# Kernel optimization log

Measured on AMD Instinct MI355X. Metric: run time of the kernel, lower is better.

## Reference

```python
import jax, jax.numpy as jnp
import numpy as np

GRID = 7
NUM_CLASSES = 80
LAMBDA_COORD = 5.0
LAMBDA_NOOBJ = 0.5
EPS_IOU = 1e-06
EPS_SQRT = 1e-06


def setup_inputs() -> dict:
    key = jax.random.key(0)
    k1, k2, k3 = jax.random.split(key, 3)
    B = 4096
    D = 10 + NUM_CLASSES
    pred = jax.random.uniform(k1, (B, GRID, GRID, D), dtype=jnp.float32)
    target = jax.random.uniform(k2, (B, GRID, GRID, D), dtype=jnp.float32)
    # confidence channel of target must be exactly 1.0 for object cells
    obj = (jax.random.uniform(k3, (B, GRID, GRID)) < 0.25).astype(jnp.float32)
    target = target.at[..., 4].set(obj)
    return {"pred": pred, "target": target}


def _iou(b1, b2):
    # b1, b2: [..., 4] boxes as (cx, cy, w, h) in image coords
    x1, y1, w1, h1 = b1[..., 0], b1[..., 1], b1[..., 2], b1[..., 3]
    x2, y2, w2, h2 = b2[..., 0], b2[..., 1], b2[..., 2], b2[..., 3]
    ix_min = jnp.maximum(x1 - w1 / 2, x2 - w2 / 2)
    iy_min = jnp.maximum(y1 - h1 / 2, y2 - h2 / 2)
    ix_max = jnp.minimum(x1 + w1 / 2, x2 + w2 / 2)
    iy_max = jnp.minimum(y1 + h1 / 2, y2 + h2 / 2)
    iw = jnp.clip(ix_max - ix_min, 0.0)
    ih = jnp.clip(iy_max - iy_min, 0.0)
    inter = iw * ih
    union = w1 * h1 + w2 * h2 - inter
    return inter / (union + EPS_IOU)


def _forward(pred, target):
    S = pred.shape[1]
    gy = jnp.arange(S, dtype=pred.dtype).reshape(1, S, 1)
    gx = jnp.arange(S, dtype=pred.dtype).reshape(1, 1, S)

    def to_img(box5):  # [B,S,S,5] cell-relative -> [B,S,S,4] image coords
        cx = (gx + box5[..., 0]) / S
        cy = (gy + box5[..., 1]) / S
        return jnp.stack([cx, cy, box5[..., 2], box5[..., 3]], axis=-1)

    box1 = pred[..., 0:5]
    box2 = pred[..., 5:10]
    tbox = target[..., 0:5]

    iou1 = _iou(to_img(box1), to_img(tbox))
    iou2 = _iou(to_img(box2), to_img(tbox))
    resp1 = iou1 > iou2  # box1 responsible if strictly greater (matches `if iou1 > iou2`)
    best = jnp.where(resp1[..., None], box1, box2)  # [B,S,S,5]

    obj = target[..., 4] == 1.0  # [B,S,S]
    objf = obj.astype(pred.dtype)
    n_obj = jnp.sum(objf)
    n_cells = jnp.asarray(pred.shape[0] * S * S, pred.dtype)

    # coord: mean-of-2 xy MSE + mean-of-2 sqrt(wh) MSE per responsible box
    dxy2 = jnp.sum((best[..., 0:2] - tbox[..., 0:2]) ** 2, axis=-1)
    swh_p = jnp.sqrt(jnp.clip(best[..., 2:4], EPS_SQRT))
    swh_t = jnp.sqrt(jnp.clip(tbox[..., 2:4], EPS_SQRT))
    dwh2 = jnp.sum((swh_p - swh_t) ** 2, axis=-1)
    coord_per = 0.5 * dxy2 + 0.5 * dwh2
    coord_loss = jnp.sum(coord_per * objf) / jnp.maximum(n_obj, 1.0)

    # confidence: obj cells -> (best_conf - 1)^2 (count 1); noobj -> lam*(c1^2 + c2^2) (count 2)
    conf_obj = (best[..., 4] - 1.0) ** 2
    conf_noobj = LAMBDA_NOOBJ * (pred[..., 4] ** 2 + pred[..., 9] ** 2)
    conf_sum = jnp.sum(jnp.where(obj, conf_obj, conf_noobj))
    conf_count = n_obj + 2.0 * (n_cells - n_obj)
    conf_loss = conf_sum / jnp.maximum(conf_count, 1.0)

    # class: mean over classes per obj cell
    class_per = jnp.mean((pred[..., 10:] - target[..., 10:]) ** 2, axis=-1)
    class_loss = jnp.sum(class_per * objf) / jnp.maximum(n_obj, 1.0)

    return LAMBDA_COORD * coord_loss + conf_loss + class_loss


def reference(pred, target):
    return _forward(pred, target)
```

## Files before the change

### kernel.cpp

```cpp
#include <hip/hip_runtime.h>

#define GRID_S 7
#define NUM_CLASSES 80
#define D_DIM 90
#define LAMBDA_COORD 5.0f
#define LAMBDA_NOOBJ 0.5f
#define EPS_IOU 1e-6f
#define EPS_SQRT 1e-6f

#define GA 630

__device__ __forceinline__ float iou_img(float cx1, float cy1, float w1, float h1,
                                         float cx2, float cy2, float w2, float h2) {
    float ixmin = fmaxf(cx1 - w1 * 0.5f, cx2 - w2 * 0.5f);
    float iymin = fmaxf(cy1 - h1 * 0.5f, cy2 - h2 * 0.5f);
    float ixmax = fminf(cx1 + w1 * 0.5f, cx2 + w2 * 0.5f);
    float iymax = fminf(cy1 + h1 * 0.5f, cy2 + h2 * 0.5f);
    float iw = fmaxf(ixmax - ixmin, 0.0f);
    float ih = fmaxf(iymax - iymin, 0.0f);
    float inter = iw * ih;
    float uni = w1 * h1 + w2 * h2 - inter;
    return inter / (uni + EPS_IOU);
}

__global__ __launch_bounds__(256) void yolo_main_kernel(
        const float* __restrict__ pred, const float* __restrict__ targ,
        float* __restrict__ part, int ncells) {
    const int tid = threadIdx.x;
    float v_obj = 0.0f, v_coord = 0.0f, v_conf = 0.0f, v_cls = 0.0f;

    if (blockIdx.x < GA) {
        const int NF4 = (ncells * D_DIM) >> 2;
        const int T = GA * 256;
        const int t = blockIdx.x * 256 + tid;
        const int phase = t % 45;
        int g = t / 45;
        const int GSTRIDE = T / 45;

        float w0[4], w1[4];
        #pragma unroll
        for (int e = 0; e < 4; ++e) {
            int fe = phase * 4 + e;
            int ce = (fe >= 90) ? 1 : 0;
            int de = fe - 90 * ce;
            float cw = (de >= 10) ? 1.0f : 0.0f;
            w0[e] = ce ? 0.0f : cw;
            w1[e] = ce ? cw : 0.0f;
        }

        const float4* p4 = (const float4*)pred;
        const float4* t4 = (const float4*)targ;
        float acc = 0.0f;
        for (int j = t; j < NF4; j += T, g += GSTRIDE) {
            float4 p = p4[j];
            float4 tv = t4[j];
            const float* ob = targ + (size_t)g * 180;
            float o0 = ob[4];
            float o1 = ob[94];
            float f0 = (o0 == 1.0f) ? 1.0f : 0.0f;
            float f1 = (o1 == 1.0f) ? 1.0f : 0.0f;
            float d0 = p.x - tv.x;
            float d1 = p.y - tv.y;
            float d2 = p.z - tv.z;
            float d3 = p.w - tv.w;
            acc = fmaf(d0 * d0, fmaf(w1[0], f1, w0[0] * f0), acc);
            acc = fmaf(d1 * d1, fmaf(w1[1], f1, w0[1] * f0), acc);
            acc = fmaf(d2 * d2, fmaf(w1[2], f1, w0[2] * f0), acc);
            acc = fmaf(d3 * d3, fmaf(w1[3], f1, w0[3] * f0), acc);
        }
        v_cls = acc * (1.0f / (float)NUM_CLASSES);
    } else {
        const int cell = (blockIdx.x - GA) * 256 + tid;
        if (cell < ncells) {
            const float2* cp2 = (const float2*)(pred + (size_t)cell * D_DIM);
            const float2* ct2 = (const float2*)(targ + (size_t)cell * D_DIM);
            float2 pA = cp2[0], pB = cp2[1], pC = cp2[2], pD = cp2[3], pE = cp2[4];
            float2 tA = ct2[0], tB = ct2[1], tC = ct2[2];

            float b1x = pA.x, b1y = pA.y, b1w = pB.x, b1h = pB.y, b1c = pC.x;
            float b2x = pC.y, b2y = pD.x, b2w = pD.y, b2h = pE.x, b2c = pE.y;
            float tbx = tA.x, tby = tA.y, tbw = tB.x, tbh = tB.y;
            float tobj = tC.x;

            const int gxy = cell % (GRID_S * GRID_S);
            const float gy = (float)(gxy / GRID_S);
            const float gx = (float)(gxy % GRID_S);
            const float invS = 1.0f / (float)GRID_S;
            float c1x = (gx + b1x) * invS, c1y = (gy + b1y) * invS;
            float c2x = (gx + b2x) * invS, c2y = (gy + b2y) * invS;
            float ctx = (gx + tbx) * invS, cty = (gy + tby) * invS;

            float iou1 = iou_img(c1x, c1y, b1w, b1h, ctx, cty, tbw, tbh);
            float iou2 = iou_img(c2x, c2y, b2w, b2h, ctx, cty, tbw, tbh);
            bool resp1 = iou1 > iou2;

            float bx = resp1 ? b1x : b2x;
            float by = resp1 ? b1y : b2y;
            float bw = resp1 ? b1w : b2w;
            float bh = resp1 ? b1h : b2h;
            float bc = resp1 ? b1c : b2c;

            bool obj = (tobj == 1.0f);
            float objf = obj ? 1.0f : 0.0f;

            float ddx = bx - tbx, ddy = by - tby;
            float dxy2 = ddx * ddx + ddy * ddy;
            float swpw = sqrtf(fmaxf(bw, EPS_SQRT));
            float swph = sqrtf(fmaxf(bh, EPS_SQRT));
            float swtw = sqrtf(fmaxf(tbw, EPS_SQRT));
            float swth = sqrtf(fmaxf(tbh, EPS_SQRT));
            float dw = swpw - swtw, dh = swph - swth;
            float dwh2 = dw * dw + dh * dh;
            float coord = 0.5f * dxy2 + 0.5f * dwh2;

            float dco = bc - 1.0f;
            float conf_obj = dco * dco;
            float conf_noobj = LAMBDA_NOOBJ * (b1c * b1c + b2c * b2c);

            v_obj = objf;
            v_coord = coord * objf;
            v_conf = obj ? conf_obj : conf_noobj;
        }
    }

    #pragma unroll
    for (int off = 32; off > 0; off >>= 1) {
        v_obj   += __shfl_down(v_obj, off, 64);
        v_coord += __shfl_down(v_coord, off, 64);
        v_conf  += __shfl_down(v_conf, off, 64);
        v_cls   += __shfl_down(v_cls, off, 64);
    }
    __shared__ float red[4][4];
    const int lane = tid & 63;
    const int wid = tid >> 6;
    if (lane == 0) {
        red[wid][0] = v_obj;
        red[wid][1] = v_coord;
        red[wid][2] = v_conf;
        red[wid][3] = v_cls;
    }
    __syncthreads();
    if (tid < 4) {
        float s = red[0][tid] + red[1][tid] + red[2][tid] + red[3][tid];
        part[(size_t)blockIdx.x * 4 + tid] = s;
    }
}

__global__ __launch_bounds__(1024) void yolo_final_kernel(
        const float* __restrict__ part, float* __restrict__ out,
        int nblocks, int ncells) {
    const int tid = threadIdx.x;
    float a0 = 0.0f, a1 = 0.0f, a2 = 0.0f, a3 = 0.0f;
    const float4* p4 = (const float4*)part;
    for (int b = tid; b < nblocks; b += 1024) {
        float4 v = p4[b];
        a0 += v.x; a1 += v.y; a2 += v.z; a3 += v.w;
    }
    #pragma unroll
    for (int off = 32; off > 0; off >>= 1) {
        a0 += __shfl_down(a0, off, 64);
        a1 += __shfl_down(a1, off, 64);
        a2 += __shfl_down(a2, off, 64);
        a3 += __shfl_down(a3, off, 64);
    }
    __shared__ float red[16][4];
    const int wid = tid >> 6;
    if ((tid & 63) == 0) {
        red[wid][0] = a0; red[wid][1] = a1; red[wid][2] = a2; red[wid][3] = a3;
    }
    __syncthreads();
    if (tid == 0) {
        float n_obj = 0.0f, coord = 0.0f, conf = 0.0f, cls = 0.0f;
        #pragma unroll
        for (int w = 0; w < 16; ++w) {
            n_obj += red[w][0]; coord += red[w][1];
            conf  += red[w][2]; cls   += red[w][3];
        }
        float n_cells = (float)ncells;
        float conf_count = n_obj + 2.0f * (n_cells - n_obj);
        float denom = fmaxf(n_obj, 1.0f);
        out[0] = LAMBDA_COORD * coord / denom + conf / fmaxf(conf_count, 1.0f) + cls / denom;
    }
}

extern "C" void kernel_launch(void* const* d_in, const int* in_sizes, int n_in,
                              void* d_out, int out_size, void* d_ws, size_t ws_size,
                              hipStream_t stream) {
    const float* pred = (const float*)d_in[0];
    const float* targ = (const float*)d_in[1];
    float* part = (float*)d_ws;
    float* out = (float*)d_out;

    const int ncells = in_sizes[0] / D_DIM;
    const int GB = (ncells + 255) / 256;
    const int nblocks = GA + GB;

    yolo_main_kernel<<<nblocks, 256, 0, stream>>>(pred, targ, part, ncells);
    yolo_final_kernel<<<1, 1024, 0, stream>>>(part, out, nblocks, ncells);
}
```

Before: 163.2 us.

## Fuse box-loss computation into streaming pass via shared-memory staging of box fields

Replaces the split grid (streaming class-loss blocks plus separate per-cell box blocks) with a single persistent grid of 1024 blocks. Each block streams windows of 5 cell-pairs with float4 loads, stages the box and target fields in double-buffered shared memory, and lets a few spare threads compute IoU and the coord/conf terms from there. This removes the second, poorly coalesced read of the box fields and the strided objectness loads. In exchange it adds a __syncthreads per window, leaves most threads idle during the box math, and handles an odd last cell serially in the final kernel.

```diff
diff --git a/kernel.cpp b/kernel.cpp
--- a/kernel.cpp
+++ b/kernel.cpp
@@ -8,7 +8,9 @@
 #define EPS_IOU 1e-6f
 #define EPS_SQRT 1e-6f
 
-#define GA 630
+#define SB 1024
+#define WIN 225
+#define GPW 5
 
 __device__ __forceinline__ float iou_img(float cx1, float cy1, float w1, float h1,
                                          float cx2, float cy2, float w2, float h2) {
@@ -23,105 +25,142 @@
     return inter / (uni + EPS_IOU);
 }
 
-__global__ __launch_bounds__(256) void yolo_main_kernel(
+__global__ __launch_bounds__(256, 4) void yolo_fused_kernel(
         const float* __restrict__ pred, const float* __restrict__ targ,
         float* __restrict__ part, int ncells) {
     const int tid = threadIdx.x;
-    float v_obj = 0.0f, v_coord = 0.0f, v_conf = 0.0f, v_cls = 0.0f;
-
-    if (blockIdx.x < GA) {
-        const int NF4 = (ncells * D_DIM) >> 2;
-        const int T = GA * 256;
-        const int t = blockIdx.x * 256 + tid;
-        const int phase = t % 45;
-        int g = t / 45;
-        const int GSTRIDE = T / 45;
-
-        float w0[4], w1[4];
-        #pragma unroll
-        for (int e = 0; e < 4; ++e) {
-            int fe = phase * 4 + e;
-            int ce = (fe >= 90) ? 1 : 0;
-            int de = fe - 90 * ce;
-            float cw = (de >= 10) ? 1.0f : 0.0f;
-            w0[e] = ce ? 0.0f : cw;
-            w1[e] = ce ? cw : 0.0f;
-        }
-
-        const float4* p4 = (const float4*)pred;
-        const float4* t4 = (const float4*)targ;
-        float acc = 0.0f;
-        for (int j = t; j < NF4; j += T, g += GSTRIDE) {
-            float4 p = p4[j];
-            float4 tv = t4[j];
-            const float* ob = targ + (size_t)g * 180;
-            float o0 = ob[4];
-            float o1 = ob[94];
-            float f0 = (o0 == 1.0f) ? 1.0f : 0.0f;
-            float f1 = (o1 == 1.0f) ? 1.0f : 0.0f;
-            float d0 = p.x - tv.x;
-            float d1 = p.y - tv.y;
-            float d2 = p.z - tv.z;
-            float d3 = p.w - tv.w;
+    const int G2 = ncells >> 1;
+    const int nwin = (G2 + GPW - 1) / GPW;
+    const int iters = (nwin + SB - 1) / SB;
+
+    const bool is_stream = tid < WIN;
+    const int q = tid % 45;
+    const int lg = tid / 45;
+
+    float w0[4], w1[4];
+    #pragma unroll
+    for (int e = 0; e < 4; ++e) {
+        int fe = q * 4 + e;
+        int ce = (fe >= 90) ? 1 : 0;
+        int de = fe - 90 * ce;
+        float cw = (de >= 10) ? 1.0f : 0.0f;
+        w0[e] = ce ? 0.0f : cw;
+        w1[e] = ce ? cw : 0.0f;
+    }
+
+    __shared__ float pbox[2][GPW][20];
+    __shared__ float tbox[2][GPW][10];
+
+    const bool is_box = (tid >= 232) && (tid < 232 + 2 * GPW);
+    const int bgid = tid - 232;
+    const int blg = bgid >> 1;
+    const int bcell = bgid & 1;
+
+    const float4* p4 = (const float4*)pred;
+    const float4* t4 = (const float4*)targ;
+
+    float acc = 0.0f, v_obj = 0.0f, v_coord = 0.0f, v_conf = 0.0f;
+
+    for (int i = 0; i < iters; ++i) {
+        const int win = i * SB + blockIdx.x;
+        const int gbase = win * GPW;
+        const int p = i & 1;
+        const int g = gbase + lg;
+        const bool v = is_stream && (g < G2);
+        float4 P, Tv;
+        if (v) {
+            const int j = win * WIN + tid;
+            P = p4[j];
+            Tv = t4[j];
+            if (q == 0) {
+                pbox[p][lg][0] = P.x; pbox[p][lg][1] = P.y;
+                pbox[p][lg][2] = P.z; pbox[p][lg][3] = P.w;
+                tbox[p][lg][0] = Tv.x; tbox[p][lg][1] = Tv.y;
+                tbox[p][lg][2] = Tv.z; tbox[p][lg][3] = Tv.w;
+            } else if (q == 1) {
+                pbox[p][lg][4] = P.x; pbox[p][lg][5] = P.y;
+                pbox[p][lg][6] = P.z; pbox[p][lg][7] = P.w;
+                tbox[p][lg][4] = Tv.x;
+            } else if (q == 2) {
+                pbox[p][lg][8] = P.x; pbox[p][lg][9] = P.y;
+            } else if (q == 22) {
+                pbox[p][lg][10] = P.z; pbox[p][lg][11] = P.w;
+                tbox[p][lg][5] = Tv.z; tbox[p][lg][6] = Tv.w;
+            } else if (q == 23) {
+                pbox[p][lg][12] = P.x; pbox[p][lg][13] = P.y;
+                pbox[p][lg][14] = P.z; pbox[p][lg][15] = P.w;
+                tbox[p][lg][7] = Tv.x; tbox[p][lg][8] = Tv.y;
+                tbox[p][lg][9] = Tv.z;
+            } else if (q == 24) {
+                pbox[p][lg][16] = P.x; pbox[p][lg][17] = P.y;
+                pbox[p][lg][18] = P.z; pbox[p][lg][19] = P.w;
+            }
+        }
+        __syncthreads();
+        if (v) {
+            float f0 = (tbox[p][lg][4] == 1.0f) ? 1.0f : 0.0f;
+            float f1 = (tbox[p][lg][9] == 1.0f) ? 1.0f : 0.0f;
+            float d0 = P.x - Tv.x, d1 = P.y - Tv.y;
+            float d2 = P.z - Tv.z, d3 = P.w - Tv.w;
             acc = fmaf(d0 * d0, fmaf(w1[0], f1, w0[0] * f0), acc);
             acc = fmaf(d1 * d1, fmaf(w1[1], f1, w0[1] * f0), acc);
             acc = fmaf(d2 * d2, fmaf(w1[2], f1, w0[2] * f0), acc);
             acc = fmaf(d3 * d3, fmaf(w1[3], f1, w0[3] * f0), acc);
         }
-        v_cls = acc * (1.0f / (float)NUM_CLASSES);
-    } else {
-        const int cell = (blockIdx.x - GA) * 256 + tid;
-        if (cell < ncells) {
-            const float2* cp2 = (const float2*)(pred + (size_t)cell * D_DIM);
-            const float2* ct2 = (const float2*)(targ + (size_t)cell * D_DIM);
-            float2 pA = cp2[0], pB = cp2[1], pC = cp2[2], pD = cp2[3], pE = cp2[4];
-            float2 tA = ct2[0], tB = ct2[1], tC = ct2[2];
-
-            float b1x = pA.x, b1y = pA.y, b1w = pB.x, b1h = pB.y, b1c = pC.x;
-            float b2x = pC.y, b2y = pD.x, b2w = pD.y, b2h = pE.x, b2c = pE.y;
-            float tbx = tA.x, tby = tA.y, tbw = tB.x, tbh = tB.y;
-            float tobj = tC.x;
-
-            const int gxy = cell % (GRID_S * GRID_S);
-            const float gy = (float)(gxy / GRID_S);
-            const float gx = (float)(gxy % GRID_S);
-            const float invS = 1.0f / (float)GRID_S;
-            float c1x = (gx + b1x) * invS, c1y = (gy + b1y) * invS;
-            float c2x = (gx + b2x) * invS, c2y = (gy + b2y) * invS;
-            float ctx = (gx + tbx) * invS, cty = (gy + tby) * invS;
-
-            float iou1 = iou_img(c1x, c1y, b1w, b1h, ctx, cty, tbw, tbh);
-            float iou2 = iou_img(c2x, c2y, b2w, b2h, ctx, cty, tbw, tbh);
-            bool resp1 = iou1 > iou2;
-
-            float bx = resp1 ? b1x : b2x;
-            float by = resp1 ? b1y : b2y;
-            float bw = resp1 ? b1w : b2w;
-            float bh = resp1 ? b1h : b2h;
-            float bc = resp1 ? b1c : b2c;
-
-            bool obj = (tobj == 1.0f);
-            float objf = obj ? 1.0f : 0.0f;
-
-            float ddx = bx - tbx, ddy = by - tby;
-            float dxy2 = ddx * ddx + ddy * ddy;
-            float swpw = sqrtf(fmaxf(bw, EPS_SQRT));
-            float swph = sqrtf(fmaxf(bh, EPS_SQRT));
-            float swtw = sqrtf(fmaxf(tbw, EPS_SQRT));
-            float swth = sqrtf(fmaxf(tbh, EPS_SQRT));
-            float dw = swpw - swtw, dh = swph - swth;
-            float dwh2 = dw * dw + dh * dh;
-            float coord = 0.5f * dxy2 + 0.5f * dwh2;
-
-            float dco = bc - 1.0f;
-            float conf_obj = dco * dco;
-            float conf_noobj = LAMBDA_NOOBJ * (b1c * b1c + b2c * b2c);
-
-            v_obj = objf;
-            v_coord = coord * objf;
-            v_conf = obj ? conf_obj : conf_noobj;
-        }
-    }
+        if (is_box) {
+            const int bg = gbase + blg;
+            if (bg < G2) {
+                const float* pb = &pbox[p][blg][bcell * 10];
+                const float* tb = &tbox[p][blg][bcell * 5];
+                float b1x = pb[0], b1y = pb[1], b1w = pb[2], b1h = pb[3], b1c = pb[4];
+                float b2x = pb[5], b2y = pb[6], b2w = pb[7], b2h = pb[8], b2c = pb[9];
+                float tbx = tb[0], tby = tb[1], tbw = tb[2], tbh = tb[3];
+                float tobj = tb[4];
+
+                const int cell = 2 * bg + bcell;
+                const int gxy = cell % (GRID_S * GRID_S);
+                const float gy = (float)(gxy / GRID_S);
+                const float gx = (float)(gxy % GRID_S);
+                const float invS = 1.0f / (float)GRID_S;
+                float c1x = (gx + b1x) * invS, c1y = (gy + b1y) * invS;
+                float c2x = (gx + b2x) * invS, c2y = (gy + b2y) * invS;
+                float ctx = (gx + tbx) * invS, cty = (gy + tby) * invS;
+
+                float iou1 = iou_img(c1x, c1y, b1w, b1h, ctx, cty, tbw, tbh);
+                float iou2 = iou_img(c2x, c2y, b2w, b2h, ctx, cty, tbw, tbh);
+                bool resp1 = iou1 > iou2;
+
+                float bx = resp1 ? b1x : b2x;
+                float by = resp1 ? b1y : b2y;
+                float bw = resp1 ? b1w : b2w;
+                float bh = resp1 ? b1h : b2h;
+                float bc = resp1 ? b1c : b2c;
+
+                bool obj = (tobj == 1.0f);
+                float objf = obj ? 1.0f : 0.0f;
+
+                float ddx = bx - tbx, ddy = by - tby;
+                float dxy2 = ddx * ddx + ddy * ddy;
+                float swpw = sqrtf(fmaxf(bw, EPS_SQRT));
+                float swph = sqrtf(fmaxf(bh, EPS_SQRT));
+                float swtw = sqrtf(fmaxf(tbw, EPS_SQRT));
+                float swth = sqrtf(fmaxf(tbh, EPS_SQRT));
+                float dw = swpw - swtw, dh = swph - swth;
+                float dwh2 = dw * dw + dh * dh;
+                float coord = 0.5f * dxy2 + 0.5f * dwh2;
+
+                float dco = bc - 1.0f;
+                float conf_obj = dco * dco;
+                float conf_noobj = LAMBDA_NOOBJ * (b1c * b1c + b2c * b2c);
+
+                v_obj += objf;
+                v_coord += coord * objf;
+                v_conf += obj ? conf_obj : conf_noobj;
+            }
+        }
+    }
+
+    float v_cls = acc * (1.0f / (float)NUM_CLASSES);
 
     #pragma unroll
     for (int off = 32; off > 0; off >>= 1) {
@@ -148,6 +187,7 @@
 
 __global__ __launch_bounds__(1024) void yolo_final_kernel(
         const float* __restrict__ part, float* __restrict__ out,
+        const float* __restrict__ pred, const float* __restrict__ targ,
         int nblocks, int ncells) {
     const int tid = threadIdx.x;
     float a0 = 0.0f, a1 = 0.0f, a2 = 0.0f, a3 = 0.0f;
@@ -176,6 +216,37 @@
             n_obj += red[w][0]; coord += red[w][1];
             conf  += red[w][2]; cls   += red[w][3];
         }
+        if (ncells & 1) {
+            const int cell = ncells - 1;
+            const float* cp = pred + (size_t)cell * D_DIM;
+            const float* ct = targ + (size_t)cell * D_DIM;
+            float objf = (ct[4] == 1.0f) ? 1.0f : 0.0f;
+            float c = 0.0f;
+            for (int k = 10; k < 90; ++k) { float d = cp[k] - ct[k]; c += d * d; }
+            cls += c * (1.0f / (float)NUM_CLASSES) * objf;
+            const int gxy = cell % (GRID_S * GRID_S);
+            const float gy = (float)(gxy / GRID_S);
+            const float gx = (float)(gxy % GRID_S);
+            const float invS = 1.0f / (float)GRID_S;
+            float c1x = (gx + cp[0]) * invS, c1y = (gy + cp[1]) * invS;
+            float c2x = (gx + cp[5]) * invS, c2y = (gy + cp[6]) * invS;
+            float ctx = (gx + ct[0]) * invS, cty = (gy + ct[1]) * invS;
+            float iou1 = iou_img(c1x, c1y, cp[2], cp[3], ctx, cty, ct[2], ct[3]);
+            float iou2 = iou_img(c2x, c2y, cp[7], cp[8], ctx, cty, ct[2], ct[3]);
+            bool r1 = iou1 > iou2;
+            float bx = r1 ? cp[0] : cp[5], by = r1 ? cp[1] : cp[6];
+            float bw = r1 ? cp[2] : cp[7], bh = r1 ? cp[3] : cp[8];
+            float bc = r1 ? cp[4] : cp[9];
+            float ddx = bx - ct[0], ddy = by - ct[1];
+            float dw = sqrtf(fmaxf(bw, EPS_SQRT)) - sqrtf(fmaxf(ct[2], EPS_SQRT));
+            float dh = sqrtf(fmaxf(bh, EPS_SQRT)) - sqrtf(fmaxf(ct[3], EPS_SQRT));
+            float coord1 = 0.5f * (ddx * ddx + ddy * ddy) + 0.5f * (dw * dw + dh * dh);
+            float dco = bc - 1.0f;
+            n_obj += objf;
+            coord += coord1 * objf;
+            conf  += (objf == 1.0f) ? dco * dco
+                                    : LAMBDA_NOOBJ * (cp[4] * cp[4] + cp[9] * cp[9]);
+        }
         float n_cells = (float)ncells;
         float conf_count = n_obj + 2.0f * (n_cells - n_obj);
         float denom = fmaxf(n_obj, 1.0f);
@@ -192,9 +263,7 @@
     float* out = (float*)d_out;
 
     const int ncells = in_sizes[0] / D_DIM;
-    const int GB = (ncells + 255) / 256;
-    const int nblocks = GA + GB;
-
-    yolo_main_kernel<<<nblocks, 256, 0, stream>>>(pred, targ, part, ncells);
-    yolo_final_kernel<<<1, 1024, 0, stream>>>(part, out, nblocks, ncells);
-}
+
+    yolo_fused_kernel<<<SB, 256, 0, stream>>>(pred, targ, part, ncells);
+    yolo_final_kernel<<<1, 1024, 0, stream>>>(part, out, pred, targ, SB, ncells);
+}
```

Measured after the change: 159.9 us. 1.02x faster.

## Gate class-loss reads on object mask via per-block compacted cell list

Applied to the files above, without the earlier changes.

Replaces the dense class-loss sweep over all pred and target data with a per-block scheme. Each thread first reads only the confidence fields of its cell. Object cells are then compacted into a shared-memory list, and threads process the listed cells, reading the class channels only for those. This aims to skip loading the class data of non-object cells, about three quarters of cells with the test inputs. The cost is that each thread reads a full 90-float row, which gives strided, poorly coalesced accesses and adds atomics and an extra block barrier.

```diff
diff --git a/kernel.cpp b/kernel.cpp
--- a/kernel.cpp
+++ b/kernel.cpp
@@ -7,8 +7,6 @@
 #define LAMBDA_NOOBJ 0.5f
 #define EPS_IOU 1e-6f
 #define EPS_SQRT 1e-6f
-
-#define GA 630
 
 __device__ __forceinline__ float iou_img(float cx1, float cy1, float w1, float h1,
                                          float cx2, float cy2, float w2, float h2) {
@@ -23,104 +21,95 @@
     return inter / (uni + EPS_IOU);
 }
 
-__global__ __launch_bounds__(256) void yolo_main_kernel(
+__global__ __launch_bounds__(256) void yolo_gated_kernel(
         const float* __restrict__ pred, const float* __restrict__ targ,
         float* __restrict__ part, int ncells) {
     const int tid = threadIdx.x;
+    const int cell = blockIdx.x * 256 + tid;
+
+    __shared__ int s_list[256];
+    __shared__ int s_count;
+    if (tid == 0) s_count = 0;
+    __syncthreads();
+
     float v_obj = 0.0f, v_coord = 0.0f, v_conf = 0.0f, v_cls = 0.0f;
 
-    if (blockIdx.x < GA) {
-        const int NF4 = (ncells * D_DIM) >> 2;
-        const int T = GA * 256;
-        const int t = blockIdx.x * 256 + tid;
-        const int phase = t % 45;
-        int g = t / 45;
-        const int GSTRIDE = T / 45;
+    bool obj = false;
+    if (cell < ncells) {
+        const float2* t2 = (const float2*)(targ + (size_t)cell * D_DIM);
+        const float2* p2 = (const float2*)(pred + (size_t)cell * D_DIM);
+        float2 tf = t2[2];
+        float2 pa = p2[2];
+        float2 pb = p2[4];
+        obj = (tf.x == 1.0f);
+        if (obj) {
+            v_obj = 1.0f;
+        } else {
+            v_conf = LAMBDA_NOOBJ * (pa.x * pa.x + pb.y * pb.y);
+        }
+    }
 
-        float w0[4], w1[4];
+    if (obj) {
+        int idx = atomicAdd(&s_count, 1);
+        s_list[idx] = cell;
+    }
+    __syncthreads();
+    const int n = s_count;
+
+    for (int k = tid; k < n; k += 256) {
+        const int c = s_list[k];
+        const float2* p2 = (const float2*)(pred + (size_t)c * D_DIM);
+        const float2* t2 = (const float2*)(targ + (size_t)c * D_DIM);
+
+        float2 pq0 = p2[0], pq1 = p2[1], pq2 = p2[2], pq3 = p2[3], pq4 = p2[4];
+        float2 tq0 = t2[0], tq1 = t2[1];
+
+        float cls0 = 0.0f, cls1 = 0.0f;
         #pragma unroll
-        for (int e = 0; e < 4; ++e) {
-            int fe = phase * 4 + e;
-            int ce = (fe >= 90) ? 1 : 0;
-            int de = fe - 90 * ce;
-            float cw = (de >= 10) ? 1.0f : 0.0f;
-            w0[e] = ce ? 0.0f : cw;
-            w1[e] = ce ? cw : 0.0f;
+        for (int j = 5; j < 45; ++j) {
+            float2 pc = p2[j];
+            float2 tc = t2[j];
+            float dx = pc.x - tc.x;
+            float dy = pc.y - tc.y;
+            cls0 = fmaf(dx, dx, cls0);
+            cls1 = fmaf(dy, dy, cls1);
         }
 
-        const float4* p4 = (const float4*)pred;
-        const float4* t4 = (const float4*)targ;
-        float acc = 0.0f;
-        for (int j = t; j < NF4; j += T, g += GSTRIDE) {
-            float4 p = p4[j];
-            float4 tv = t4[j];
-            const float* ob = targ + (size_t)g * 180;
-            float o0 = ob[4];
-            float o1 = ob[94];
-            float f0 = (o0 == 1.0f) ? 1.0f : 0.0f;
-            float f1 = (o1 == 1.0f) ? 1.0f : 0.0f;
-            float d0 = p.x - tv.x;
-            float d1 = p.y - tv.y;
-            float d2 = p.z - tv.z;
-            float d3 = p.w - tv.w;
-            acc = fmaf(d0 * d0, fmaf(w1[0], f1, w0[0] * f0), acc);
-            acc = fmaf(d1 * d1, fmaf(w1[1], f1, w0[1] * f0), acc);
-            acc = fmaf(d2 * d2, fmaf(w1[2], f1, w0[2] * f0), acc);
-            acc = fmaf(d3 * d3, fmaf(w1[3], f1, w0[3] * f0), acc);
-        }
-        v_cls = acc * (1.0f / (float)NUM_CLASSES);
-    } else {
-        const int cell = (blockIdx.x - GA) * 256 + tid;
-        if (cell < ncells) {
-            const float2* cp2 = (const float2*)(pred + (size_t)cell * D_DIM);
-            const float2* ct2 = (const float2*)(targ + (size_t)cell * D_DIM);
-            float2 pA = cp2[0], pB = cp2[1], pC = cp2[2], pD = cp2[3], pE = cp2[4];
-            float2 tA = ct2[0], tB = ct2[1], tC = ct2[2];
+        float b1x = pq0.x, b1y = pq0.y, b1w = pq1.x, b1h = pq1.y, b1c = pq2.x;
+        float b2x = pq2.y, b2y = pq3.x, b2w = pq3.y, b2h = pq4.x, b2c = pq4.y;
+        float tbx = tq0.x, tby = tq0.y, tbw = tq1.x, tbh = tq1.y;
 
-            float b1x = pA.x, b1y = pA.y, b1w = pB.x, b1h = pB.y, b1c = pC.x;
-            float b2x = pC.y, b2y = pD.x, b2w = pD.y, b2h = pE.x, b2c = pE.y;
-            float tbx = tA.x, tby = tA.y, tbw = tB.x, tbh = tB.y;
-            float tobj = tC.x;
+        const int gxy = c % (GRID_S * GRID_S);
+        const float gy = (float)(gxy / GRID_S);
+        const float gx = (float)(gxy % GRID_S);
+        const float invS = 1.0f / (float)GRID_S;
+        float c1x = (gx + b1x) * invS, c1y = (gy + b1y) * invS;
+        float c2x = (gx + b2x) * invS, c2y = (gy + b2y) * invS;
+        float ctx = (gx + tbx) * invS, cty = (gy + tby) * invS;
 
-            const int gxy = cell % (GRID_S * GRID_S);
-            const float gy = (float)(gxy / GRID_S);
-            const float gx = (float)(gxy % GRID_S);
-            const float invS = 1.0f / (float)GRID_S;
-            float c1x = (gx + b1x) * invS, c1y = (gy + b1y) * invS;
-            float c2x = (gx + b2x) * invS, c2y = (gy + b2y) * invS;
-            float ctx = (gx + tbx) * invS, cty = (gy + tby) * invS;
+        float iou1 = iou_img(c1x, c1y, b1w, b1h, ctx, cty, tbw, tbh);
+        float iou2 = iou_img(c2x, c2y, b2w, b2h, ctx, cty, tbw, tbh);
+        bool resp1 = iou1 > iou2;
 
-            float iou1 = iou_img(c1x, c1y, b1w, b1h, ctx, cty, tbw, tbh);
-            float iou2 = iou_img(c2x, c2y, b2w, b2h, ctx, cty, tbw, tbh);
-            bool resp1 = iou1 > iou2;
+        float bx = resp1 ? b1x : b2x;
+        float by = resp1 ? b1y : b2y;
+        float bw = resp1 ? b1w : b2w;
+        float bh = resp1 ? b1h : b2h;
+        float bc = resp1 ? b1c : b2c;
 
-            float bx = resp1 ? b1x : b2x;
-            float by = resp1 ? b1y : b2y;
-            float bw = resp1 ? b1w : b2w;
-            float bh = resp1 ? b1h : b2h;
-            float bc = resp1 ? b1c : b2c;
+        float ddx = bx - tbx, ddy = by - tby;
+        float dxy2 = ddx * ddx + ddy * ddy;
+        float swpw = sqrtf(fmaxf(bw, EPS_SQRT));
+        float swph = sqrtf(fmaxf(bh, EPS_SQRT));
+        float swtw = sqrtf(fmaxf(tbw, EPS_SQRT));
+        float swth = sqrtf(fmaxf(tbh, EPS_SQRT));
+        float dw = swpw - swtw, dh = swph - swth;
+        float dwh2 = dw * dw + dh * dh;
 
-            bool obj = (tobj == 1.0f);
-            float objf = obj ? 1.0f : 0.0f;
-
-            float ddx = bx - tbx, ddy = by - tby;
-            float dxy2 = ddx * ddx + ddy * ddy;
-            float swpw = sqrtf(fmaxf(bw, EPS_SQRT));
-            float swph = sqrtf(fmaxf(bh, EPS_SQRT));
-            float swtw = sqrtf(fmaxf(tbw, EPS_SQRT));
-            float swth = sqrtf(fmaxf(tbh, EPS_SQRT));
-            float dw = swpw - swtw, dh = swph - swth;
-            float dwh2 = dw * dw + dh * dh;
-            float coord = 0.5f * dxy2 + 0.5f * dwh2;
-
-            float dco = bc - 1.0f;
-            float conf_obj = dco * dco;
-            float conf_noobj = LAMBDA_NOOBJ * (b1c * b1c + b2c * b2c);
-
-            v_obj = objf;
-            v_coord = coord * objf;
-            v_conf = obj ? conf_obj : conf_noobj;
-        }
+        v_coord += 0.5f * dxy2 + 0.5f * dwh2;
+        float dco = bc - 1.0f;
+        v_conf += dco * dco;
+        v_cls += (cls0 + cls1) * (1.0f / (float)NUM_CLASSES);
     }
 
     #pragma unroll
@@ -192,9 +181,8 @@
     float* out = (float*)d_out;
 
     const int ncells = in_sizes[0] / D_DIM;
-    const int GB = (ncells + 255) / 256;
-    const int nblocks = GA + GB;
+    const int nblocks = (ncells + 255) / 256;
 
-    yolo_main_kernel<<<nblocks, 256, 0, stream>>>(pred, targ, part, ncells);
+    yolo_gated_kernel<<<nblocks, 256, 0, stream>>>(pred, targ, part, ncells);
     yolo_final_kernel<<<1, 1024, 0, stream>>>(part, out, nblocks, ncells);
 }
```

After: 150.8 us. 7.6% less time.
